# Kernel optimization log

Hardware: AMD Instinct MI355X
Metric: run time of the kernel (lower is better)

## Reference

```python
import jax, jax.numpy as jnp
import numpy as np

B, N, D, H = 4, 2048, 1024, 64

def setup_inputs() -> dict:
    key = jax.random.key(0)
    ks = jax.random.split(key, 7)
    s = D ** -0.5  # torch Linear default init scale ~ U(-1/sqrt(fan_in), ...); scale randn similarly
    return {
        "x":  jax.random.normal(ks[0], (B, N, D), dtype=jnp.float32),
        "Wq": jax.random.normal(ks[1], (D, H), dtype=jnp.float32) * s,
        "bq": jax.random.normal(ks[2], (H,), dtype=jnp.float32) * s,
        "Wk": jax.random.normal(ks[3], (D, H), dtype=jnp.float32) * s,
        "bk": jax.random.normal(ks[4], (H,), dtype=jnp.float32) * s,
        "Wv": jax.random.normal(ks[5], (D, H), dtype=jnp.float32) * s,
        "bv": jax.random.normal(ks[6], (H,), dtype=jnp.float32) * s,
    }

def reference(x, Wq, bq, Wk, bk, Wv, bv):
    head_size = Wq.shape[1]
    q = x @ Wq + bq          # [B, N, H]
    k = x @ Wk + bk          # [B, N, H]
    v = x @ Wv + bv          # [B, N, H]
    scores = jnp.einsum("bid,bjd->bij", q, k)        # [B, N, N]
    # faithful to torch: keep upper triangle (col >= row), then mask exact zeros to -inf
    scores = jnp.triu(scores)
    scores = jnp.where(scores == 0, -jnp.inf, scores)
    attn = jax.nn.softmax(scores * (head_size ** -0.5), axis=-1)  # [B, N, N]
    # out = (V^T @ attn)^T  ==  attn^T @ V
    out = jnp.einsum("bji,bjh->bih", attn, v)         # [B, N, H]
    return out
```

## Files before the change

kernel.cpp:

```cpp
#include <hip/hip_runtime.h>
#include <math.h>

constexpr int kN = 2048;
constexpr int kD = 1024;

typedef __attribute__((ext_vector_type(8))) short bf16x8;
typedef __attribute__((ext_vector_type(4))) short bf16x4;
typedef __attribute__((ext_vector_type(4))) float f32x4;

#define MFMA(a, b, c) __builtin_amdgcn_mfma_f32_16x16x32_bf16(a, b, c, 0, 0, 0)

__device__ __forceinline__ short f2bf(float f) {
    unsigned u = __float_as_uint(f);
    u += 0x7fff + ((u >> 16) & 1);
    return (short)(u >> 16);
}
__device__ __forceinline__ float bf2f(short s) {
    return __uint_as_float(((unsigned)(unsigned short)s) << 16);
}

__device__ __forceinline__ void g2l(void* lds, const void* g, int nbytes, int t) {
    int lane = t & 63, w = t >> 6;
    for (int base = w * 1024; base < nbytes; base += 4096) {
        if (base + lane * 16 < nbytes) {
            __builtin_amdgcn_global_load_lds(
                (const __attribute__((address_space(1))) void*)((const char*)g + base + lane * 16),
                (__attribute__((address_space(3))) void*)((char*)lds + base),
                16, 0, 0);
        }
    }
}

__global__ __launch_bounds__(256) void prep_kernel(
        const float* __restrict__ Wq, const float* __restrict__ Wk,
        const float* __restrict__ Wv, const float* __restrict__ bq,
        const float* __restrict__ bk, const float* __restrict__ bv,
        short* __restrict__ Wt, float* __restrict__ bcat)
{
    int tid = blockIdx.x * 256 + threadIdx.x;
    int stride = gridDim.x * 256;
    for (int e = tid; e < 16 * 12 * 2 * 512; e += stride) {
        int kc = e / 12288;
        int rem = e - kc * 12288;
        int nt = rem >> 10;
        int r2 = rem & 1023;
        int f = r2 >> 9;
        int r3 = r2 & 511;
        int q8 = r3 >> 7;
        int l15 = (r3 >> 3) & 15;
        int el = r3 & 7;
        int n = nt * 16 + l15;
        int d = kc * 64 + f * 32 + q8 * 8 + el;
        float wv = (n < 64) ? Wq[d * 64 + n]
                 : (n < 128) ? Wk[d * 64 + (n - 64)]
                 : Wv[d * 64 + (n - 128)];
        Wt[e] = f2bf(wv);
    }
    if (tid < 192)
        bcat[tid] = (tid < 64) ? bq[tid] : (tid < 128) ? bk[tid - 64] : bv[tid - 128];
}

constexpr int XP = 1032;

__global__ __launch_bounds__(256) void qkv_kernel(
        const float* __restrict__ x, const short* __restrict__ Wt,
        const float* __restrict__ bcat,
        short* __restrict__ gq, short* __restrict__ gk, short* __restrict__ vt)
{
    __shared__ __align__(16) short xs[16 * XP];
    const int t = threadIdx.x;
    const int w = t >> 6, lane = t & 63, l15 = lane & 15, q8 = lane >> 4;
    const int m0 = blockIdx.x * 16;

    {
        int row = t >> 4, c4 = (t & 15) * 4;
        const float* xr = x + (size_t)(m0 + row) * kD;
        #pragma unroll
        for (int cc = 0; cc < 16; ++cc) {
            float4 xv = *(const float4*)&xr[cc * 64 + c4];
            bf16x4 pk = {f2bf(xv.x), f2bf(xv.y), f2bf(xv.z), f2bf(xv.w)};
            *(bf16x4*)&xs[row * XP + cc * 64 + c4] = pk;
        }
    }
    __syncthreads();

    f32x4 acc[3];
    #pragma unroll
    for (int ct = 0; ct < 3; ++ct) acc[ct] = (f32x4){0.f, 0.f, 0.f, 0.f};

    #pragma unroll 4
    for (int kc = 0; kc < 16; ++kc) {
        bf16x8 a0 = *(const bf16x8*)&xs[l15 * XP + kc * 64 + q8 * 8];
        bf16x8 a1 = *(const bf16x8*)&xs[l15 * XP + kc * 64 + 32 + q8 * 8];
        #pragma unroll
        for (int ct = 0; ct < 3; ++ct) {
            int nt = w * 3 + ct;
            const short* bp = Wt + ((size_t)(kc * 12 + nt) * 2) * 512 + lane * 8;
            bf16x8 b0 = *(const bf16x8*)bp;
            bf16x8 b1 = *(const bf16x8*)(bp + 512);
            acc[ct] = MFMA(a0, b0, acc[ct]);
            acc[ct] = MFMA(a1, b1, acc[ct]);
        }
    }

    const int bz = m0 >> 11;
    const int jt = (m0 & 2047) >> 6;
    const int jb = m0 & 63;
    #pragma unroll
    for (int ct = 0; ct < 3; ++ct) {
        int nb2 = w * 48 + ct * 16;
        int n = nb2 + l15;
        float bias = bcat[n];
        if (nb2 < 64) {
            #pragma unroll
            for (int r = 0; r < 4; ++r)
                gq[(size_t)(m0 + q8 * 4 + r) * 72 + n] = f2bf(acc[ct][r] + bias);
        } else if (nb2 < 128) {
            #pragma unroll
            for (int r = 0; r < 4; ++r)
                gk[(size_t)(m0 + q8 * 4 + r) * 72 + (n - 64)] = f2bf(acc[ct][r] + bias);
        } else {
            int h = n - 128;
            bf16x4 pk = {f2bf(acc[ct][0] + bias), f2bf(acc[ct][1] + bias),
                         f2bf(acc[ct][2] + bias), f2bf(acc[ct][3] + bias)};
            *(bf16x4*)&vt[((size_t)((bz * 32 + jt) * 64 + h)) * 72 + jb + q8 * 4] = pk;
        }
    }
}

__global__ __launch_bounds__(256) void stats_kernel(
        const short* __restrict__ gq, const short* __restrict__ gk,
        float* __restrict__ l2)
{
    __shared__ __align__(16) short qsm[64 * 72];
    __shared__ __align__(16) short ksm[2][64 * 72];
    const int t = threadIdx.x;
    const int w = t >> 6, lane = t & 63, l15 = lane & 15, q8 = lane >> 4;
    const int b = blockIdx.x;
    const int ic = b & 3, bz = (b >> 2) & 3, jt = b >> 4;
    const int j0 = jt * 64;
    const int ilo = ic * 512, ihi = ilo + 512;
    const int istart = (j0 > ilo) ? j0 : ilo;
    const int count = (istart < ihi) ? ((ihi - istart) >> 6) : 0;

    float lloc[4] = {0.f, 0.f, 0.f, 0.f};

    if (count > 0) {
        g2l(qsm, gq + (size_t)(bz * kN + j0) * 72, 64 * 144, t);
        g2l(ksm[0], gk + (size_t)(bz * kN + istart) * 72, 64 * 144, t);
        __syncthreads();
        int jrow = 16 * w + l15;
        bf16x8 a0 = *(const bf16x8*)&qsm[jrow * 72 + q8 * 8];
        bf16x8 a1 = *(const bf16x8*)&qsm[jrow * 72 + 32 + q8 * 8];

        for (int idx = 0; idx < count; ++idx) {
            const int cur = idx & 1;
            if (idx + 1 < count)
                g2l(ksm[cur ^ 1],
                    gk + (size_t)(bz * kN + istart + (idx + 1) * 64) * 72, 64 * 144, t);
            const int i0 = istart + idx * 64;
            #pragma unroll
            for (int it = 0; it < 4; ++it) {
                int irow = it * 16 + l15;
                bf16x8 b0 = *(const bf16x8*)&ksm[cur][irow * 72 + q8 * 8];
                bf16x8 b1 = *(const bf16x8*)&ksm[cur][irow * 72 + 32 + q8 * 8];
                f32x4 s = (f32x4){0.f, 0.f, 0.f, 0.f};
                s = MFMA(a0, b0, s);
                s = MFMA(a1, b1, s);
                int ig = i0 + it * 16 + l15;
                #pragma unroll
                for (int r = 0; r < 4; ++r) {
                    int jg = j0 + 16 * w + q8 * 4 + r;
                    float sv = s[r];
                    float e = __expf(sv * 0.125f);
                    lloc[r] += ((ig >= jg) && (sv != 0.0f)) ? e : 0.0f;
                }
            }
            __syncthreads();
        }
    }
    #pragma unroll
    for (int off = 1; off < 16; off <<= 1)
        #pragma unroll
        for (int r = 0; r < 4; ++r)
            lloc[r] += __shfl_xor(lloc[r], off);
    if (l15 == 0) {
        #pragma unroll
        for (int r = 0; r < 4; ++r)
            l2[ic * 8192 + bz * kN + j0 + 16 * w + q8 * 4 + r] = lloc[r];
    }
}

__global__ __launch_bounds__(256) void vscale_kernel(
        short* __restrict__ vt, const float* __restrict__ l2)
{
    __shared__ float rsm[64];
    const int g = blockIdx.x, t = threadIdx.x;
    if (t < 64) {
        int j = (g >> 5) * kN + (g & 31) * 64 + t;
        float l = l2[j] + l2[8192 + j] + l2[16384 + j] + l2[24576 + j];
        rsm[t] = (l > 0.f) ? 1.0f / l : 0.0f;
    }
    __syncthreads();
    const int h = t >> 2, c0 = (t & 3) * 16;
    size_t base = ((size_t)g * 64 + h) * 72 + c0;
    #pragma unroll
    for (int bb = 0; bb < 2; ++bb) {
        bf16x8 v = *(bf16x8*)&vt[base + bb * 8];
        bf16x8 o;
        #pragma unroll
        for (int e = 0; e < 8; ++e)
            o[e] = f2bf(bf2f(v[e]) * rsm[c0 + bb * 8 + e]);
        *(bf16x8*)&vt[base + bb * 8] = o;
    }
}

__global__ __launch_bounds__(256) void out_kernel(
        const short* __restrict__ gq, const short* __restrict__ gk,
        const short* __restrict__ vt, float* __restrict__ part)
{
    __shared__ __align__(16) short ksm[64 * 72];
    __shared__ __align__(16) short qsm[2][64 * 72];
    __shared__ __align__(16) short vsm[2][64 * 72];
    __shared__ __align__(16) short psm[64 * 72];
    const int t = threadIdx.x;
    const int w = t >> 6, lane = t & 63, l15 = lane & 15, q8 = lane >> 4;
    const int b = blockIdx.x;
    const int jc = b & 3, bz = (b >> 2) & 3, it = b >> 4;
    const int i0 = it * 64;
    const int jlo = jc * 512;
    const int jhi = (jlo + 512 < i0 + 64) ? (jlo + 512) : (i0 + 64);
    const int count = (jlo < jhi) ? ((jhi - jlo) >> 6) : 0;

    f32x4 oacc[4];
    #pragma unroll
    for (int i = 0; i < 4; ++i) oacc[i] = (f32x4){0.f, 0.f, 0.f, 0.f};

    if (count > 0) {
        g2l(ksm, gk + (size_t)(bz * kN + i0) * 72, 64 * 144, t);
        g2l(qsm[0], gq + (size_t)(bz * kN + jlo) * 72, 64 * 144, t);
        g2l(vsm[0], vt + (size_t)((bz * 32 + (jlo >> 6)) * 64) * 72, 64 * 144, t);
        __syncthreads();

        for (int idx = 0; idx < count; ++idx) {
            const int cur = idx & 1, nb = cur ^ 1;
            const int j0s = jlo + idx * 64;
            if (idx + 1 < count) {
                g2l(qsm[nb], gq + (size_t)(bz * kN + j0s + 64) * 72, 64 * 144, t);
                g2l(vsm[nb], vt + (size_t)((bz * 32 + ((j0s + 64) >> 6)) * 64) * 72,
                    64 * 144, t);
            }
            int jrow = 16 * w + l15;
            bf16x8 a0 = *(const bf16x8*)&qsm[cur][jrow * 72 + q8 * 8];
            bf16x8 a1 = *(const bf16x8*)&qsm[cur][jrow * 72 + 32 + q8 * 8];
            #pragma unroll
            for (int itile = 0; itile < 4; ++itile) {
                int irow = itile * 16 + l15;
                bf16x8 b0 = *(const bf16x8*)&ksm[irow * 72 + q8 * 8];
                bf16x8 b1 = *(const bf16x8*)&ksm[irow * 72 + 32 + q8 * 8];
                f32x4 sv4 = (f32x4){0.f, 0.f, 0.f, 0.f};
                sv4 = MFMA(a0, b0, sv4);
                sv4 = MFMA(a1, b1, sv4);
                int ig = i0 + itile * 16 + l15;
                bf16x4 pk;
                #pragma unroll
                for (int r = 0; r < 4; ++r) {
                    int jg = j0s + 16 * w + q8 * 4 + r;
                    float sv = sv4[r];
                    float p = ((ig >= jg) && (sv != 0.0f)) ? __expf(sv * 0.125f) : 0.0f;
                    pk[r] = f2bf(p);
                }
                *(bf16x4*)&psm[(itile * 16 + l15) * 72 + 16 * w + q8 * 4] = pk;
            }
            __syncthreads();

            bf16x8 pa0 = *(const bf16x8*)&psm[(16 * w + l15) * 72 + q8 * 8];
            bf16x8 pa1 = *(const bf16x8*)&psm[(16 * w + l15) * 72 + 32 + q8 * 8];
            #pragma unroll
            for (int ht = 0; ht < 4; ++ht) {
                int vrow = ht * 16 + l15;
                bf16x8 vb0 = *(const bf16x8*)&vsm[cur][vrow * 72 + q8 * 8];
                bf16x8 vb1 = *(const bf16x8*)&vsm[cur][vrow * 72 + 32 + q8 * 8];
                oacc[ht] = MFMA(pa0, vb0, oacc[ht]);
                oacc[ht] = MFMA(pa1, vb1, oacc[ht]);
            }
            __syncthreads();
        }
    }
    size_t base = ((size_t)(jc * 4 + bz) * kN + i0) * 64;
    #pragma unroll
    for (int ht = 0; ht < 4; ++ht)
        #pragma unroll
        for (int r = 0; r < 4; ++r)
            part[base + (size_t)(16 * w + q8 * 4 + r) * 64 + ht * 16 + l15] = oacc[ht][r];
}

__global__ __launch_bounds__(256) void reduce_kernel(
        const float* __restrict__ part, float* __restrict__ out)
{
    int idx = blockIdx.x * 256 + threadIdx.x;
    const float4* p = (const float4*)part;
    float4 a = p[idx];
    float4 b = p[idx + 131072];
    float4 c = p[idx + 262144];
    float4 d = p[idx + 393216];
    float4 r;
    r.x = a.x + b.x + c.x + d.x;
    r.y = a.y + b.y + c.y + d.y;
    r.z = a.z + b.z + c.z + d.z;
    r.w = a.w + b.w + c.w + d.w;
    ((float4*)out)[idx] = r;
}

extern "C" void kernel_launch(void* const* d_in, const int* in_sizes, int n_in,
                              void* d_out, int out_size, void* d_ws, size_t ws_size,
                              hipStream_t stream)
{
    const float* x  = (const float*)d_in[0];
    const float* Wq = (const float*)d_in[1];
    const float* bq = (const float*)d_in[2];
    const float* Wk = (const float*)d_in[3];
    const float* bk = (const float*)d_in[4];
    const float* Wv = (const float*)d_in[5];
    const float* bv = (const float*)d_in[6];
    float* out = (float*)d_out;

    char* base = (char*)d_ws;
    short* Wt   = (short*)(base);
    float* bcat = (float*)(base + 393216);
    short* gq   = (short*)(base + 394240);
    short* gk   = (short*)(base + 1573888);
    short* vt   = (short*)(base + 2753536);
    float* l2   = (float*)(base + 3933184);
    float* part = (float*)(base + 4064256);

    prep_kernel<<<256, 256, 0, stream>>>(Wq, Wk, Wv, bq, bk, bv, Wt, bcat);
    qkv_kernel<<<512, 256, 0, stream>>>(x, Wt, bcat, gq, gk, vt);
    stats_kernel<<<512, 256, 0, stream>>>(gq, gk, l2);
    vscale_kernel<<<128, 256, 0, stream>>>(vt, l2);
    out_kernel<<<512, 256, 0, stream>>>(gq, gk, vt, part);
    reduce_kernel<<<512, 256, 0, stream>>>(part, out);
}
```

Before: 126.6 us.

## Fuse V normalization into out kernel and keep Q/K operands in registers

Removes the separate vscale kernel and instead applies the per-column 1/l normalization to the probabilities inside out_kernel, with the reciprocals loaded into shared memory at block start. Q and K MFMA operands are now loaded directly from global memory into registers, with next-tile Q prefetched, so their LDS staging disappears. Exp is computed through exp2 with a folded constant, and fully unmasked tiles skip the per-element causal comparison. This saves a launch and an extra read/write pass over V, and cuts LDS traffic, at the cost of more registers and an extra multiply per probability.

```diff
diff --git a/kernel.cpp b/kernel.cpp
--- a/kernel.cpp
+++ b/kernel.cpp
@@ -1,5 +1,4 @@
 #include <hip/hip_runtime.h>
-#include <math.h>
 
 constexpr int kN = 2048;
 constexpr int kD = 1024;
@@ -9,14 +8,14 @@
 typedef __attribute__((ext_vector_type(4))) float f32x4;
 
 #define MFMA(a, b, c) __builtin_amdgcn_mfma_f32_16x16x32_bf16(a, b, c, 0, 0, 0)
+
+constexpr float kExpC = 0.18033688011112042f;
+#define EXP8(sv) __builtin_amdgcn_exp2f((sv) * kExpC)
 
 __device__ __forceinline__ short f2bf(float f) {
     unsigned u = __float_as_uint(f);
     u += 0x7fff + ((u >> 16) & 1);
     return (short)(u >> 16);
-}
-__device__ __forceinline__ float bf2f(short s) {
-    return __uint_as_float(((unsigned)(unsigned short)s) << 16);
 }
 
 __device__ __forceinline__ void g2l(void* lds, const void* g, int nbytes, int t) {
@@ -132,7 +131,6 @@
         const short* __restrict__ gq, const short* __restrict__ gk,
         float* __restrict__ l2)
 {
-    __shared__ __align__(16) short qsm[64 * 72];
     __shared__ __align__(16) short ksm[2][64 * 72];
     const int t = threadIdx.x;
     const int w = t >> 6, lane = t & 63, l15 = lane & 15, q8 = lane >> 4;
@@ -146,12 +144,11 @@
     float lloc[4] = {0.f, 0.f, 0.f, 0.f};
 
     if (count > 0) {
-        g2l(qsm, gq + (size_t)(bz * kN + j0) * 72, 64 * 144, t);
+        const short* qp = gq + (size_t)(bz * kN + j0 + 16 * w + l15) * 72 + q8 * 8;
+        bf16x8 a0 = *(const bf16x8*)qp;
+        bf16x8 a1 = *(const bf16x8*)(qp + 32);
         g2l(ksm[0], gk + (size_t)(bz * kN + istart) * 72, 64 * 144, t);
         __syncthreads();
-        int jrow = 16 * w + l15;
-        bf16x8 a0 = *(const bf16x8*)&qsm[jrow * 72 + q8 * 8];
-        bf16x8 a1 = *(const bf16x8*)&qsm[jrow * 72 + 32 + q8 * 8];
 
         for (int idx = 0; idx < count; ++idx) {
             const int cur = idx & 1;
@@ -168,12 +165,19 @@
                 s = MFMA(a0, b0, s);
                 s = MFMA(a1, b1, s);
                 int ig = i0 + it * 16 + l15;
-                #pragma unroll
-                for (int r = 0; r < 4; ++r) {
-                    int jg = j0 + 16 * w + q8 * 4 + r;
-                    float sv = s[r];
-                    float e = __expf(sv * 0.125f);
-                    lloc[r] += ((ig >= jg) && (sv != 0.0f)) ? e : 0.0f;
+                if (i0 + it * 16 >= j0 + 16 * w + 15) {
+                    #pragma unroll
+                    for (int r = 0; r < 4; ++r) {
+                        float sv = s[r];
+                        lloc[r] += (sv != 0.0f) ? EXP8(sv) : 0.0f;
+                    }
+                } else {
+                    #pragma unroll
+                    for (int r = 0; r < 4; ++r) {
+                        int jg = j0 + 16 * w + q8 * 4 + r;
+                        float sv = s[r];
+                        lloc[r] += ((ig >= jg) && (sv != 0.0f)) ? EXP8(sv) : 0.0f;
+                    }
                 }
             }
             __syncthreads();
@@ -191,38 +195,14 @@
     }
 }
 
-__global__ __launch_bounds__(256) void vscale_kernel(
-        short* __restrict__ vt, const float* __restrict__ l2)
-{
-    __shared__ float rsm[64];
-    const int g = blockIdx.x, t = threadIdx.x;
-    if (t < 64) {
-        int j = (g >> 5) * kN + (g & 31) * 64 + t;
-        float l = l2[j] + l2[8192 + j] + l2[16384 + j] + l2[24576 + j];
-        rsm[t] = (l > 0.f) ? 1.0f / l : 0.0f;
-    }
-    __syncthreads();
-    const int h = t >> 2, c0 = (t & 3) * 16;
-    size_t base = ((size_t)g * 64 + h) * 72 + c0;
-    #pragma unroll
-    for (int bb = 0; bb < 2; ++bb) {
-        bf16x8 v = *(bf16x8*)&vt[base + bb * 8];
-        bf16x8 o;
-        #pragma unroll
-        for (int e = 0; e < 8; ++e)
-            o[e] = f2bf(bf2f(v[e]) * rsm[c0 + bb * 8 + e]);
-        *(bf16x8*)&vt[base + bb * 8] = o;
-    }
-}
-
 __global__ __launch_bounds__(256) void out_kernel(
         const short* __restrict__ gq, const short* __restrict__ gk,
-        const short* __restrict__ vt, float* __restrict__ part)
-{
-    __shared__ __align__(16) short ksm[64 * 72];
-    __shared__ __align__(16) short qsm[2][64 * 72];
+        const short* __restrict__ vt, const float* __restrict__ l2,
+        float* __restrict__ part)
+{
     __shared__ __align__(16) short vsm[2][64 * 72];
     __shared__ __align__(16) short psm[64 * 72];
+    __shared__ __align__(16) float rsm[512];
     const int t = threadIdx.x;
     const int w = t >> 6, lane = t & 63, l15 = lane & 15, q8 = lane >> 4;
     const int b = blockIdx.x;
@@ -232,43 +212,69 @@
     const int jhi = (jlo + 512 < i0 + 64) ? (jlo + 512) : (i0 + 64);
     const int count = (jlo < jhi) ? ((jhi - jlo) >> 6) : 0;
 
+    #pragma unroll
+    for (int jj = t; jj < 512; jj += 256) {
+        int j = bz * kN + jlo + jj;
+        float l = l2[j] + l2[8192 + j] + l2[16384 + j] + l2[24576 + j];
+        rsm[jj] = (l > 0.f) ? 1.0f / l : 0.0f;
+    }
+
     f32x4 oacc[4];
     #pragma unroll
     for (int i = 0; i < 4; ++i) oacc[i] = (f32x4){0.f, 0.f, 0.f, 0.f};
 
     if (count > 0) {
-        g2l(ksm, gk + (size_t)(bz * kN + i0) * 72, 64 * 144, t);
-        g2l(qsm[0], gq + (size_t)(bz * kN + jlo) * 72, 64 * 144, t);
+        bf16x8 kb0[4], kb1[4];
+        #pragma unroll
+        for (int itile = 0; itile < 4; ++itile) {
+            const short* kp = gk + (size_t)(bz * kN + i0 + itile * 16 + l15) * 72 + q8 * 8;
+            kb0[itile] = *(const bf16x8*)kp;
+            kb1[itile] = *(const bf16x8*)(kp + 32);
+        }
         g2l(vsm[0], vt + (size_t)((bz * 32 + (jlo >> 6)) * 64) * 72, 64 * 144, t);
+        const short* qp = gq + (size_t)(bz * kN + jlo + 16 * w + l15) * 72 + q8 * 8;
+        bf16x8 qa0 = *(const bf16x8*)qp;
+        bf16x8 qa1 = *(const bf16x8*)(qp + 32);
         __syncthreads();
 
         for (int idx = 0; idx < count; ++idx) {
             const int cur = idx & 1, nb = cur ^ 1;
             const int j0s = jlo + idx * 64;
-            if (idx + 1 < count) {
-                g2l(qsm[nb], gq + (size_t)(bz * kN + j0s + 64) * 72, 64 * 144, t);
+            const bool more = (idx + 1 < count);
+            bf16x8 qn0, qn1;
+            if (more) {
                 g2l(vsm[nb], vt + (size_t)((bz * 32 + ((j0s + 64) >> 6)) * 64) * 72,
                     64 * 144, t);
+                const short* qn =
+                    gq + (size_t)(bz * kN + j0s + 64 + 16 * w + l15) * 72 + q8 * 8;
+                qn0 = *(const bf16x8*)qn;
+                qn1 = *(const bf16x8*)(qn + 32);
             }
-            int jrow = 16 * w + l15;
-            bf16x8 a0 = *(const bf16x8*)&qsm[cur][jrow * 72 + q8 * 8];
-            bf16x8 a1 = *(const bf16x8*)&qsm[cur][jrow * 72 + 32 + q8 * 8];
+            f32x4 rl4 = *(const f32x4*)&rsm[(j0s - jlo) + 16 * w + q8 * 4];
+
             #pragma unroll
             for (int itile = 0; itile < 4; ++itile) {
-                int irow = itile * 16 + l15;
-                bf16x8 b0 = *(const bf16x8*)&ksm[irow * 72 + q8 * 8];
-                bf16x8 b1 = *(const bf16x8*)&ksm[irow * 72 + 32 + q8 * 8];
-                f32x4 sv4 = (f32x4){0.f, 0.f, 0.f, 0.f};
-                sv4 = MFMA(a0, b0, sv4);
-                sv4 = MFMA(a1, b1, sv4);
+                f32x4 s = (f32x4){0.f, 0.f, 0.f, 0.f};
+                s = MFMA(qa0, kb0[itile], s);
+                s = MFMA(qa1, kb1[itile], s);
                 int ig = i0 + itile * 16 + l15;
                 bf16x4 pk;
-                #pragma unroll
-                for (int r = 0; r < 4; ++r) {
-                    int jg = j0s + 16 * w + q8 * 4 + r;
-                    float sv = sv4[r];
-                    float p = ((ig >= jg) && (sv != 0.0f)) ? __expf(sv * 0.125f) : 0.0f;
-                    pk[r] = f2bf(p);
+                if (i0 + itile * 16 >= j0s + 16 * w + 15) {
+                    #pragma unroll
+                    for (int r = 0; r < 4; ++r) {
+                        float sv = s[r];
+                        float p = (sv != 0.0f) ? EXP8(sv) * rl4[r] : 0.0f;
+                        pk[r] = f2bf(p);
+                    }
+                } else {
+                    #pragma unroll
+                    for (int r = 0; r < 4; ++r) {
+                        int jg = j0s + 16 * w + q8 * 4 + r;
+                        float sv = s[r];
+                        float p = ((ig >= jg) && (sv != 0.0f))
+                                  ? EXP8(sv) * rl4[r] : 0.0f;
+                        pk[r] = f2bf(p);
+                    }
                 }
                 *(bf16x4*)&psm[(itile * 16 + l15) * 72 + 16 * w + q8 * 4] = pk;
             }
@@ -285,6 +291,7 @@
                 oacc[ht] = MFMA(pa1, vb1, oacc[ht]);
             }
             __syncthreads();
+            if (more) { qa0 = qn0; qa1 = qn1; }
         }
     }
     size_t base = ((size_t)(jc * 4 + bz) * kN + i0) * 64;
@@ -337,7 +344,6 @@
     prep_kernel<<<256, 256, 0, stream>>>(Wq, Wk, Wv, bq, bk, bv, Wt, bcat);
     qkv_kernel<<<512, 256, 0, stream>>>(x, Wt, bcat, gq, gk, vt);
     stats_kernel<<<512, 256, 0, stream>>>(gq, gk, l2);
-    vscale_kernel<<<128, 256, 0, stream>>>(vt, l2);
-    out_kernel<<<512, 256, 0, stream>>>(gq, gk, vt, part);
+    out_kernel<<<512, 256, 0, stream>>>(gq, gk, vt, l2, part);
     reduce_kernel<<<512, 256, 0, stream>>>(part, out);
 }
```

After: 122.6 us. -3.1%, faster.
